# Kernel tuning notes

Measured on AMD Instinct MI355X. Metric: run time of the kernel, lower is better.

## Reference

```python
import jax, jax.numpy as jnp
import numpy as np

B, C, R = 1024, 256, 7          # batch, channels, ROI feature map res
PATCH, DIL = 16, 2              # correlation patch size, dilation_patch
REP = 1024                      # representation_size
FLAT = PATCH * PATCH * R * R    # 12544 = fc1 input dim


def setup_inputs() -> dict:
    key = jax.random.key(0)
    k = jax.random.split(key, 8)
    return {
        "patch1": jax.random.normal(k[0], (B, C, R, R), dtype=jnp.float32),
        "patch2": jax.random.normal(k[1], (B, C, R, R), dtype=jnp.float32),
        "W1": jax.random.normal(k[2], (REP, FLAT), dtype=jnp.float32) * 0.01,
        "b1": jnp.zeros((REP,), dtype=jnp.float32),
        "W2": jax.random.normal(k[3], (REP, REP), dtype=jnp.float32) * 0.02,
        "b2": jnp.zeros((REP,), dtype=jnp.float32),
        "W3": jax.random.normal(k[4], (4, REP), dtype=jnp.float32) * 0.02,
        "b3": jnp.zeros((4,), dtype=jnp.float32),
    }


def _correlate(p1, p2):
    """SpatialCorrelationSampler(patch_size=16, dilation_patch=2), kernel=1, stride=1.
    out[b, pi, pj, i, j] = sum_c p1[b,c,i,j] * p2[b,c, i+(pi-8)*2, j+(pj-8)*2]
    (zero outside bounds). Returns [B, PATCH*PATCH, R, R]."""
    pad = (PATCH // 2) * DIL  # 16; displacements span [-16, 14]
    p2p = jnp.pad(p2, ((0, 0), (0, 0), (pad, pad), (pad, pad)))  # [B,C,39,39]
    outs = []
    for pi in range(PATCH):
        for pj in range(PATCH):
            # shifted window: row offset (pi-8)*2 + pad = 2*pi, same for cols
            win = p2p[:, :, DIL * pi:DIL * pi + R, DIL * pj:DIL * pj + R]
            outs.append(jnp.einsum('bchw,bchw->bhw', p1, win))
    return jnp.stack(outs, axis=1)  # [B, 256, 7, 7] -> matches torch flatten order


def reference(patch1, patch2, W1, b1, W2, b2, W3, b3):
    x = _correlate(patch1, patch2).reshape(patch1.shape[0], -1)  # [B, 12544]
    x = jax.nn.relu(x @ W1.T + b1)
    x = jax.nn.relu(x @ W2.T + b2)
    pred_boxes = x @ W3.T + b3  # [B, 4]
    return pred_boxes
```

## Files before the change

kernel.cpp:

```cpp
#include <hip/hip_runtime.h>

#define BATCH 1024
#define RR    49
#define SP    12544
#define KVALID 625
#define KPAD   640
#define REP_N  1024

typedef __attribute__((ext_vector_type(4))) float f32x4;
typedef __attribute__((ext_vector_type(8))) short s16x8;

__device__ __forceinline__ unsigned short f2bf_rne(float f) {
    unsigned int u = __float_as_uint(f);
    unsigned int r = u + 0x7FFFu + ((u >> 16) & 1u);
    return (unsigned short)(r >> 16);
}
__device__ __forceinline__ float bf2f(unsigned short h) {
    return __uint_as_float(((unsigned int)h) << 16);
}
__device__ __forceinline__ void split2(float v, unsigned short& h, unsigned short& l) {
    h = f2bf_rne(v);
    l = f2bf_rne(v - bf2f(h));
}
__device__ __forceinline__ unsigned int cvtpk_bf16(float a, float b) {
    unsigned int r;
    asm("v_cvt_pk_bf16_f32 %0, %1, %2" : "=v"(r) : "v"(a), "v"(b));
    return r;
}
__device__ __forceinline__ void cvt8(const float* v, s16x8& hv, s16x8& lv) {
    unsigned int* hp = (unsigned int*)&hv;
    unsigned int* lp = (unsigned int*)&lv;
    #pragma unroll
    for (int i = 0; i < 4; ++i) {
        float v0 = v[2 * i], v1 = v[2 * i + 1];
        unsigned int ph = cvtpk_bf16(v0, v1);
        float h0 = __uint_as_float(ph << 16);
        float h1 = __uint_as_float(ph & 0xFFFF0000u);
        unsigned int pl = cvtpk_bf16(v0 - h0, v1 - h1);
        hp[i] = ph; lp[i] = pl;
    }
}

__device__ __forceinline__ void dec25(int u, int& i, int& d) {
    int ii = (u >= 4) + (u >= 7) + (u >= 11) + (u >= 14) + (u >= 18) + (u >= 21);
    int cum = (7 * ii + 1) >> 1;
    i = ii;
    d = 2 * (u - cum) + (ii & 1);
}
__device__ __forceinline__ int enc25(int i, int d) {
    return ((7 * i + 1) >> 1) + ((d - (i & 1)) >> 1);
}

__device__ __forceinline__ int kflat_of(int a) {
    int ar = a / 25, ac = a % 25;
    int i, dy, j, dx;
    dec25(ar, i, dy);
    dec25(ac, j, dx);
    int pi = (dy + 16 - i) >> 1;
    int pj = (dx + 16 - j) >> 1;
    return (pi * 16 + pj) * 49 + i * 7 + j;
}

#define MM(d, a, b) d = __builtin_amdgcn_mfma_f32_16x16x32_bf16(a, b, d, 0, 0, 0)

__global__ __launch_bounds__(256) void corr_prep_kernel(
    const float* __restrict__ p1, const float* __restrict__ p2,
    const float* __restrict__ W1, const float* __restrict__ W2,
    unsigned short* __restrict__ xh, unsigned short* __restrict__ xl,
    unsigned short* __restrict__ w1h, unsigned short* __restrict__ w1l,
    unsigned short* __restrict__ w2h, unsigned short* __restrict__ w2l)
{
    __shared__ float4 Tb[2][2][448];
    __shared__ unsigned short SXh[KPAD];
    __shared__ unsigned short SXl[KPAD];

    const int bid = blockIdx.x;
    const int t   = threadIdx.x;

    bool isCorr = false;
    int cid = 0, pid = 0;
    if (bid < 2048) {
        if ((bid & 1) == 0) { isCorr = true; cid = bid >> 1; }
        else                { pid = bid >> 1; }
    } else {
        pid = 1024 + (bid - 2048);
    }

    if (!isCorr) {
        if (pid < 2560) {
            int idx = pid * 256 + t;
            int n = idx / KPAD, a = idx - n * KPAD;
            float v = 0.f;
            if (a < KVALID) v = W1[(size_t)n * SP + kflat_of(a)];
            unsigned short h, l;
            split2(v, h, l);
            w1h[idx] = h; w1l[idx] = l;
        } else {
            int idx = ((pid - 2560) * 256 + t) * 4;
            float4 v = *(const float4*)&W2[idx];
            unsigned short h0, l0, h1, l1, h2, l2, h3, l3;
            split2(v.x, h0, l0); split2(v.y, h1, l1);
            split2(v.z, h2, l2); split2(v.w, h3, l3);
            *(ushort4*)&w2h[idx] = make_ushort4(h0, h1, h2, h3);
            *(ushort4*)&w2l[idx] = make_ushort4(l0, l1, l2, l3);
        }
        return;
    }

    const float* P1 = p1 + (size_t)cid * SP;
    const float* P2 = p2 + (size_t)cid * SP;

    const int wv   = t >> 6;
    const int lane = t & 63;
    const int fr   = lane & 15;
    const int fg   = (lane >> 4) * 8;

    const int ci = wv >> 1, cj = wv & 1;
    const int nj = 4 - cj;
    const int clsN = (4 - ci) * nj;
    const int pr = (fr < clsN) ? fr : 0;
    const int sPos = (2 * (pr / nj) + ci) * 7 + (2 * (pr % nj) + cj);

    const float* PS = (wv < 2) ? P1 : P2;
    const int tens  = wv >> 1;
    const int start = (wv & 1) * 4;
    const int nb    = (wv & 1) ? 3 : 4;

    #define STAGE(buf, hc)                                                     \
        do {                                                                   \
            const int off_ = (hc) * 1568;                                      \
            float4* T_ = &Tb[(buf)][tens][0];                                  \
            _Pragma("unroll")                                                  \
            for (int j_ = 0; j_ < 4; ++j_) {                                   \
                if (j_ < nb) {                                                 \
                    const int bq_  = start + j_;                               \
                    const int src_ = min(bq_ * 64 + lane, 391);                \
                    __builtin_amdgcn_global_load_lds(                          \
                        (const __attribute__((address_space(1))) unsigned int*)\
                            (PS + off_ + src_ * 4),                            \
                        (__attribute__((address_space(3))) unsigned int*)      \
                            (T_ + bq_ * 64),                                   \
                        16, 0, 0);                                             \
                }                                                              \
            }                                                                  \
        } while (0)

    for (int i = t; i < KPAD; i += 256) { SXh[i] = 0; SXl[i] = 0; }

    STAGE(0, 0);

    f32x4 acc = {};
    int cur = 0;
    #pragma unroll
    for (int hc = 0; hc < 8; ++hc) {
        __syncthreads();
        if (hc < 7) STAGE(cur ^ 1, hc + 1);

        const float* Tf1 = (const float*)&Tb[cur][0][0];
        const float* Tf2 = (const float*)&Tb[cur][1][0];
        const int kb = fg * RR + sPos;
        float av[8], bv[8];
        #pragma unroll
        for (int i = 0; i < 8; ++i) {
            av[i] = Tf1[kb + i * RR];
            bv[i] = Tf2[kb + i * RR];
        }
        s16x8 ah, al, bh, bl;
        cvt8(av, ah, al);
        cvt8(bv, bh, bl);
        MM(acc, ah, bh);
        MM(acc, ah, bl);
        MM(acc, al, bh);
        cur ^= 1;
    }
    #undef STAGE

    const int arow = (lane >> 4) * 4;
    if (fr < clsN) {
        const int dy = 2 * (fr / nj) + ci;
        const int dx = 2 * (fr % nj) + cj;
        #pragma unroll
        for (int r = 0; r < 4; ++r) {
            const int rowp = arow + r;
            if (rowp < clsN) {
                const int i1 = 2 * (rowp / nj) + ci;
                const int j1 = 2 * (rowp % nj) + cj;
                const int aidx = enc25(i1, dy) * 25 + enc25(j1, dx);
                unsigned short hh, ll;
                split2(acc[r], hh, ll);
                SXh[aidx] = hh; SXl[aidx] = ll;
            }
        }
    }
    __syncthreads();

    unsigned int* rh = (unsigned int*)(xh + (size_t)cid * KPAD);
    unsigned int* rl = (unsigned int*)(xl + (size_t)cid * KPAD);
    const unsigned int* sh = (const unsigned int*)SXh;
    const unsigned int* sl = (const unsigned int*)SXl;
    for (int i = t; i < KPAD / 2; i += 256) { rh[i] = sh[i]; rl[i] = sl[i]; }
}

template<bool SPLIT_OUT>
__global__ __launch_bounds__(256) void gemm_mfma(
    const unsigned short* __restrict__ Xh, const unsigned short* __restrict__ Xl, int ldx,
    const unsigned short* __restrict__ Wh, const unsigned short* __restrict__ Wl, int ldw,
    const float* __restrict__ bias, int K,
    float* __restrict__ Yf, unsigned short* __restrict__ Yh, unsigned short* __restrict__ Yl,
    int ldy)
{
    __shared__ unsigned short As[2][64][72];
    __shared__ unsigned short Bs[2][32][72];

    const int t = threadIdx.x;
    const int m_base = blockIdx.y * 64;
    const int n_base = blockIdx.x * 32;

    const int trow = t >> 2;
    const int tc   = (t & 3) * 8;
    const int trB  = t >> 3;
    const int tcB  = (t & 7) * 8;

    const unsigned short* xh_p = Xh + (size_t)(m_base + trow) * ldx + tc;
    const unsigned short* xl_p = Xl + (size_t)(m_base + trow) * ldx + tc;
    const unsigned short* wh_p = Wh + (size_t)(n_base + trB) * ldw + tcB;
    const unsigned short* wl_p = Wl + (size_t)(n_base + trB) * ldw + tcB;

    const int wv   = t >> 6;
    const int lane = t & 63;
    const int wr = (wv >> 1) * 32;
    const int wc = (wv & 1) * 16;
    const int fr = lane & 15;
    const int fg = (lane >> 4) * 8;

    f32x4 acc0 = {}, acc1 = {};

    for (int k0 = 0; k0 < K; k0 += 64) {
        s16x8 vxh0 = *(const s16x8*)(xh_p + k0);
        s16x8 vxh1 = *(const s16x8*)(xh_p + k0 + 32);
        s16x8 vxl0 = *(const s16x8*)(xl_p + k0);
        s16x8 vxl1 = *(const s16x8*)(xl_p + k0 + 32);
        s16x8 vwh  = *(const s16x8*)(wh_p + k0);
        s16x8 vwl  = *(const s16x8*)(wl_p + k0);
        __syncthreads();
        *(s16x8*)&As[0][trow][tc]      = vxh0;
        *(s16x8*)&As[0][trow][tc + 32] = vxh1;
        *(s16x8*)&As[1][trow][tc]      = vxl0;
        *(s16x8*)&As[1][trow][tc + 32] = vxl1;
        *(s16x8*)&Bs[0][trB][tcB]      = vwh;
        *(s16x8*)&Bs[1][trB][tcB]      = vwl;
        __syncthreads();

        #pragma unroll
        for (int ks = 0; ks < 2; ++ks) {
            const int ko = ks * 32 + fg;
            s16x8 ah0 = *(const s16x8*)&As[0][wr + fr][ko];
            s16x8 ah1 = *(const s16x8*)&As[0][wr + 16 + fr][ko];
            s16x8 al0 = *(const s16x8*)&As[1][wr + fr][ko];
            s16x8 al1 = *(const s16x8*)&As[1][wr + 16 + fr][ko];
            s16x8 bh  = *(const s16x8*)&Bs[0][wc + fr][ko];
            s16x8 bl  = *(const s16x8*)&Bs[1][wc + fr][ko];

            MM(acc0, ah0, bh); MM(acc0, ah0, bl); MM(acc0, al0, bh);
            MM(acc1, ah1, bh); MM(acc1, ah1, bl); MM(acc1, al1, bh);
        }
    }

    const int arow = (lane >> 4) * 4;
    const int col = n_base + wc + fr;
    const float bv = bias[col];
    #pragma unroll
    for (int mf = 0; mf < 2; ++mf) {
        const f32x4 a = mf == 0 ? acc0 : acc1;
        #pragma unroll
        for (int r = 0; r < 4; ++r) {
            const int row = m_base + wr + mf * 16 + arow + r;
            float v = fmaxf(a[r] + bv, 0.f);
            if (SPLIT_OUT) {
                unsigned short h, l;
                split2(v, h, l);
                Yh[(size_t)row * ldy + col] = h;
                Yl[(size_t)row * ldy + col] = l;
            } else {
                Yf[(size_t)row * ldy + col] = v;
            }
        }
    }
}

__global__ __launch_bounds__(256) void head_kernel(
    const float* __restrict__ h2, const float* __restrict__ W3,
    const float* __restrict__ b3, float* __restrict__ out)
{
    const int b = blockIdx.x;
    const int t = threadIdx.x;
    const float* row = h2 + (size_t)b * REP_N;

    float a0 = 0.f, a1 = 0.f, a2 = 0.f, a3 = 0.f;
    for (int k = t; k < REP_N; k += 256) {
        float x = row[k];
        a0 = fmaf(x, W3[k],             a0);
        a1 = fmaf(x, W3[REP_N + k],     a1);
        a2 = fmaf(x, W3[2 * REP_N + k], a2);
        a3 = fmaf(x, W3[3 * REP_N + k], a3);
    }
    #pragma unroll
    for (int off = 32; off > 0; off >>= 1) {
        a0 += __shfl_down(a0, off);
        a1 += __shfl_down(a1, off);
        a2 += __shfl_down(a2, off);
        a3 += __shfl_down(a3, off);
    }
    __shared__ float red[4][4];
    int wid = t >> 6, lane = t & 63;
    if (lane == 0) { red[wid][0] = a0; red[wid][1] = a1; red[wid][2] = a2; red[wid][3] = a3; }
    __syncthreads();
    if (t < 4) {
        out[b * 4 + t] = red[0][t] + red[1][t] + red[2][t] + red[3][t] + b3[t];
    }
}

extern "C" void kernel_launch(void* const* d_in, const int* in_sizes, int n_in,
                              void* d_out, int out_size, void* d_ws, size_t ws_size,
                              hipStream_t stream) {
    const float* p1 = (const float*)d_in[0];
    const float* p2 = (const float*)d_in[1];
    const float* W1 = (const float*)d_in[2];
    const float* b1 = (const float*)d_in[3];
    const float* W2 = (const float*)d_in[4];
    const float* b2 = (const float*)d_in[5];
    const float* W3 = (const float*)d_in[6];
    const float* b3 = (const float*)d_in[7];
    float* out = (float*)d_out;

    char* ws = (char*)d_ws;
    unsigned short* xh  = (unsigned short*)(ws + 0);
    unsigned short* xl  = (unsigned short*)(ws + 1310720);
    unsigned short* w1h = (unsigned short*)(ws + 2621440);
    unsigned short* w1l = (unsigned short*)(ws + 3932160);
    float*          h2  = (float*)(ws + 0);
    unsigned short* h1h = (unsigned short*)(ws + 5242880);
    unsigned short* h1l = (unsigned short*)(ws + 7340032);
    unsigned short* w2h = (unsigned short*)(ws + 9437184);
    unsigned short* w2l = (unsigned short*)(ws + 11534336);

    corr_prep_kernel<<<4608, 256, 0, stream>>>(
        p1, p2, W1, W2, xh, xl, w1h, w1l, w2h, w2l);

    gemm_mfma<true><<<dim3(32, 16), 256, 0, stream>>>(
        xh, xl, KPAD, w1h, w1l, KPAD, b1, KPAD,
        (float*)nullptr, h1h, h1l, REP_N);

    gemm_mfma<false><<<dim3(32, 16), 256, 0, stream>>>(
        h1h, h1l, REP_N, w2h, w2l, REP_N, b2, REP_N,
        h2, (unsigned short*)nullptr, (unsigned short*)nullptr, REP_N);

    head_kernel<<<BATCH, 256, 0, stream>>>(h2, W3, b3, out);
}
```

Baseline: 62.59 us.

## Prefetch two stages ahead with explicit vmcnt waits and write correlation output directly

The correlation kernel now issues the first two LDS stage loads up front and, inside the loop, waits on a partial vmcnt count before a raw s_barrier. It refills the buffer just consumed two stages ahead, so global-to-LDS loads overlap more of the compute. The LDS staging buffers for the packed bf16 output are removed: results are scattered straight to global memory and only the pad tail is zeroed. This depends on the hand-coded vmcnt counts matching the number of loads each wave issues, and it trades coalesced 32-bit stores for scattered 16-bit global stores.

```diff
diff --git a/kernel.cpp b/kernel.cpp
--- a/kernel.cpp
+++ b/kernel.cpp
@@ -71,8 +71,6 @@
     unsigned short* __restrict__ w2h, unsigned short* __restrict__ w2l)
 {
     __shared__ float4 Tb[2][2][448];
-    __shared__ unsigned short SXh[KPAD];
-    __shared__ unsigned short SXl[KPAD];
 
     const int bid = blockIdx.x;
     const int t   = threadIdx.x;
@@ -145,17 +143,22 @@
             }                                                                  \
         } while (0)
 
-    for (int i = t; i < KPAD; i += 256) { SXh[i] = 0; SXl[i] = 0; }
-
     STAGE(0, 0);
+    STAGE(1, 1);
 
     f32x4 acc = {};
-    int cur = 0;
     #pragma unroll
     for (int hc = 0; hc < 8; ++hc) {
-        __syncthreads();
-        if (hc < 7) STAGE(cur ^ 1, hc + 1);
-
+        if (hc < 7) {
+            if (wv & 1) asm volatile("s_waitcnt vmcnt(3)" ::: "memory");
+            else        asm volatile("s_waitcnt vmcnt(4)" ::: "memory");
+        } else {
+            asm volatile("s_waitcnt vmcnt(0)" ::: "memory");
+        }
+        __builtin_amdgcn_s_barrier();
+        __builtin_amdgcn_sched_barrier(0);
+
+        const int cur = hc & 1;
         const float* Tf1 = (const float*)&Tb[cur][0][0];
         const float* Tf2 = (const float*)&Tb[cur][1][0];
         const int kb = fg * RR + sPos;
@@ -171,10 +174,19 @@
         MM(acc, ah, bh);
         MM(acc, ah, bl);
         MM(acc, al, bh);
-        cur ^= 1;
+
+        __builtin_amdgcn_sched_barrier(0);
+        __builtin_amdgcn_s_barrier();
+        if (hc < 6) STAGE(cur, hc + 2);
     }
     #undef STAGE
 
+    unsigned short* rh = xh + (size_t)cid * KPAD;
+    unsigned short* rl = xl + (size_t)cid * KPAD;
+    if (t < KPAD - KVALID) {
+        rh[KVALID + t] = 0;
+        rl[KVALID + t] = 0;
+    }
     const int arow = (lane >> 4) * 4;
     if (fr < clsN) {
         const int dy = 2 * (fr / nj) + ci;
@@ -188,17 +200,10 @@
                 const int aidx = enc25(i1, dy) * 25 + enc25(j1, dx);
                 unsigned short hh, ll;
                 split2(acc[r], hh, ll);
-                SXh[aidx] = hh; SXl[aidx] = ll;
+                rh[aidx] = hh; rl[aidx] = ll;
             }
         }
     }
-    __syncthreads();
-
-    unsigned int* rh = (unsigned int*)(xh + (size_t)cid * KPAD);
-    unsigned int* rl = (unsigned int*)(xl + (size_t)cid * KPAD);
-    const unsigned int* sh = (const unsigned int*)SXh;
-    const unsigned int* sl = (const unsigned int*)SXl;
-    for (int i = t; i < KPAD / 2; i += 256) { rh[i] = sh[i]; rl[i] = sl[i]; }
 }
 
 template<bool SPLIT_OUT>
```

New measurement: 60.21 us, median of 3. 3.8% less time.
